# Performance work log

Hardware: AMD Instinct MI355X
Metric: run time of the kernel (lower is better)

Reference implementation:

```python
import jax, jax.numpy as jnp
import numpy as np

S, B, I, H = 512, 64, 512, 512

def setup_inputs() -> dict:
    key = jax.random.key(0)
    ks = jax.random.split(key, 10)
    inp = {
        'x':    jax.random.normal(ks[0], (S, B, I), dtype=jnp.float32),
        'W_xi': jax.random.normal(ks[1], (H, I), dtype=jnp.float32) * (1.0 / np.sqrt(I)),
        'W_hi': jax.random.normal(ks[2], (H, H), dtype=jnp.float32) * (1.0 / np.sqrt(H)),
        'b_i':  jax.random.normal(ks[3], (H,), dtype=jnp.float32),
        'W_xc': jax.random.normal(ks[4], (H, I), dtype=jnp.float32) * (1.0 / np.sqrt(I)),
        'W_hc': jax.random.normal(ks[5], (H, H), dtype=jnp.float32) * (1.0 / np.sqrt(H)),
        'b_c':  jax.random.normal(ks[6], (H,), dtype=jnp.float32),
        'W_xo': jax.random.normal(ks[7], (H, I), dtype=jnp.float32) * (1.0 / np.sqrt(I)),
        'W_ho': jax.random.normal(ks[8], (H, H), dtype=jnp.float32) * (1.0 / np.sqrt(H)),
        'b_o':  jax.random.normal(ks[9], (H,), dtype=jnp.float32),
    }
    return inp

def reference(x, W_xi, W_hi, b_i, W_xc, W_hc, b_c, W_xo, W_ho, b_o):
    seq_len, batch, _ = x.shape
    hidden = W_hi.shape[0]
    # Precompute all input-to-gate projections in one pass: [S,B,H] each
    xi = jnp.einsum('sbi,hi->sbh', x, W_xi)
    xc = jnp.einsum('sbi,hi->sbh', x, W_xc)
    xo = jnp.einsum('sbi,hi->sbh', x, W_xo)

    h0 = jnp.zeros((batch, hidden), dtype=x.dtype)
    c0 = jnp.zeros((batch, hidden), dtype=x.dtype)

    def step(carry, xs):
        h, c = carry
        xi_t, xc_t, xo_t = xs
        i_t = jax.nn.sigmoid(xi_t + h @ W_hi.T + b_i)
        c_hat = jnp.tanh(xc_t + h @ W_hc.T + b_c)
        c = (1.0 - i_t) * c + i_t * c_hat  # coupled forget gate f = 1 - i
        o_t = jax.nn.sigmoid(xo_t + h @ W_ho.T + b_o)
        h = o_t * jnp.tanh(c)
        return (h, c), h

    (h_t, c_t), output = jax.lax.scan(step, (h0, c0), (xi, xc, xo))
    # output: [S,B,H] (time-major, matching torch after transposes)
    return output, h_t, c_t
```

## Files before the change

kernel.cpp:

```cpp
#include <hip/hip_runtime.h>
#include <math.h>

#define SEQ   512
#define BATCH 64
#define HID   512
#define NROW  1536
#define XROW_FLOATS ((size_t)SEQ * NROW * BATCH)
#define HBUF_QWORDS (2 * BATCH * HID)
#define SBH ((size_t)SEQ * BATCH * HID)

__device__ __forceinline__ float sigf(float x) {
    return 1.f / (1.f + __expf(-x));
}
__device__ __forceinline__ float tanh_fast(float x) {
    float ax = fabsf(x);
    float e = __expf(-2.f * ax);
    float r = (1.f - e) / (1.f + e);
    return copysignf(r, x);
}
template <int CTRL>
__device__ __forceinline__ float dpp_add(float v) {
    int x = __builtin_amdgcn_update_dpp(0, __builtin_bit_cast(int, v),
                                        CTRL, 0xf, 0xf, true);
    return v + __builtin_bit_cast(float, x);
}

__global__ __launch_bounds__(256) void xproj_kernel(
    const float* __restrict__ x, const float* __restrict__ Wxi,
    const float* __restrict__ Wxc, const float* __restrict__ Wxo,
    float* __restrict__ xrow)
{
    const int tid = threadIdx.x, lane = tid & 63, wv = tid >> 6;
    const int t = blockIdx.x;
    const int bq = lane & 15;
    const int rq = lane >> 4;
    const float* xb = x + ((size_t)t * 64 + 4 * bq) * 512;

    for (int mm = 0; mm < 12; ++mm) {
        const int R0 = mm * 128 + wv * 32 + rq * 8;
        const int g = R0 >> 9, j0 = R0 & 511;
        const float* wsrc = (g == 0) ? Wxi : ((g == 1) ? Wxc : Wxo);
        const float* wp = wsrc + (size_t)j0 * 512;

        float acc[8][4];
        #pragma unroll
        for (int r = 0; r < 8; ++r)
            #pragma unroll
            for (int j = 0; j < 4; ++j) acc[r][j] = 0.f;

        for (int k4 = 0; k4 < 128; ++k4) {
            float4 xv[4];
            #pragma unroll
            for (int j = 0; j < 4; ++j)
                xv[j] = *(const float4*)(xb + j * 512 + k4 * 4);
            #pragma unroll
            for (int r = 0; r < 8; ++r) {
                const float4 w4 = *(const float4*)(wp + (size_t)r * 512 + k4 * 4);
                #pragma unroll
                for (int j = 0; j < 4; ++j)
                    acc[r][j] += w4.x * xv[j].x + w4.y * xv[j].y
                               + w4.z * xv[j].z + w4.w * xv[j].w;
            }
        }
        #pragma unroll
        for (int r = 0; r < 8; ++r)
            *(float4*)(xrow + ((size_t)t * NROW + R0 + r) * 64 + 4 * bq) =
                make_float4(acc[r][0], acc[r][1], acc[r][2], acc[r][3]);
    }
}

#define HPAD 10
#define H_FLOATS (512 * HPAD)
__global__ __launch_bounds__(512, 2) void scan_kernel(
    const float* __restrict__ xrow,
    const float* __restrict__ Whi, const float* __restrict__ Whc, const float* __restrict__ Who,
    const float* __restrict__ bi, const float* __restrict__ bc, const float* __restrict__ bo,
    unsigned long long* __restrict__ hbuf, float* __restrict__ out)
{
    extern __shared__ float lds[];
    float* hlds = lds;
    float* gbuf = lds + H_FLOATS;
    float* biasL = gbuf + 384;

    const int tid = threadIdx.x, lane = tid & 63;
    const int gid = blockIdx.x & 7;
    const int m   = blockIdx.x >> 3;
    const int rg  = tid >> 5, ks = tid & 31;

    float w3r[16][3];
    #pragma unroll
    for (int r = 0; r < 3; ++r) {
        const int rho = rg * 3 + r;
        const int g = rho >> 4, jloc = rho & 15;
        const float* wsrc = (g == 0) ? Whi : ((g == 1) ? Whc : Who);
        const float* wp = wsrc + (size_t)(m * 16 + jloc) * 512 + ks;
        #pragma unroll
        for (int i = 0; i < 16; ++i) w3r[i][r] = wp[32 * i];
    }
    if (tid < 48) {
        const int g = tid >> 4, jloc = tid & 15;
        const float* bb = (g == 0) ? bi : ((g == 1) ? bc : bo);
        biasL[tid] = bb[m * 16 + jloc];
    }

    const int ejl = tid & 15, eb = tid >> 4;
    const int jg  = m * 16 + ejl;
    const int bg  = gid * 8 + eb;
    float creg = 0.f;

    if (tid < 128) hlds[jg * HPAD + eb] = 0.f;
    __syncthreads();

    const bool own_k = ((tid >> 4) == m);

    for (int t = 0; t < SEQ; ++t) {
        float xr0 = 0.f, xr1 = 0.f, xr2 = 0.f;
        if (tid < 128) {
            const size_t base = ((size_t)t * NROW + jg) * 64 + bg;
            xr0 = xrow[base];
            xr1 = xrow[base + (size_t)512 * 64];
            xr2 = xrow[base + (size_t)1024 * 64];
        }

        if (!own_k) {
            const unsigned long long* hsrc =
                hbuf + (size_t)(t & 1) * (BATCH * HID) + (size_t)gid * 8 * 512 + tid;
            const unsigned tgt = (unsigned)t;
            unsigned long long hv[8];
            #pragma unroll
            for (int q = 0; q < 8; ++q)
                hv[q] = __hip_atomic_load(hsrc + (size_t)q * 512, __ATOMIC_RELAXED,
                                          __HIP_MEMORY_SCOPE_AGENT);
            unsigned pend = 0xffu;
            while (pend) {
                unsigned np = 0;
                #pragma unroll
                for (int q = 0; q < 8; ++q) {
                    if ((pend >> q) & 1) {
                        if ((unsigned)(hv[q] >> 32) >= tgt) {
                            hlds[tid * HPAD + q] =
                                __builtin_bit_cast(float, (unsigned)hv[q]);
                        } else np |= 1u << q;
                    }
                }
                if (np) {
                    #pragma unroll
                    for (int q = 0; q < 8; ++q)
                        if ((np >> q) & 1)
                            hv[q] = __hip_atomic_load(hsrc + (size_t)q * 512,
                                                      __ATOMIC_RELAXED,
                                                      __HIP_MEMORY_SCOPE_AGENT);
                    __builtin_amdgcn_s_sleep(1);
                }
                pend = np;
            }
        }
        __syncthreads();

        float acc[3][8];
        #pragma unroll
        for (int r = 0; r < 3; ++r)
            #pragma unroll
            for (int b = 0; b < 8; ++b) acc[r][b] = 0.f;

        {
            const float* hb = hlds + ks * HPAD;
            #pragma unroll
            for (int i = 0; i < 16; ++i) {
                float hv2[8];
                *(float2*)&hv2[0] = *(const float2*)(hb + i * (32 * HPAD) + 0);
                *(float2*)&hv2[2] = *(const float2*)(hb + i * (32 * HPAD) + 2);
                *(float2*)&hv2[4] = *(const float2*)(hb + i * (32 * HPAD) + 4);
                *(float2*)&hv2[6] = *(const float2*)(hb + i * (32 * HPAD) + 6);
                #pragma unroll
                for (int r = 0; r < 3; ++r)
                    #pragma unroll
                    for (int b = 0; b < 8; ++b)
                        acc[r][b] += w3r[i][r] * hv2[b];
            }
            #pragma unroll
            for (int r = 0; r < 3; ++r)
                #pragma unroll
                for (int b = 0; b < 8; ++b) {
                    float v = acc[r][b];
                    v = dpp_add<0x121>(v);
                    v = dpp_add<0x122>(v);
                    v = dpp_add<0x124>(v);
                    v = dpp_add<0x128>(v);
                    v = dpp_add<0x142>(v);
                    acc[r][b] = v;
                }
            if (lane == 16 || lane == 48) {
                #pragma unroll
                for (int r = 0; r < 3; ++r) {
                    float* gp = gbuf + (rg * 3 + r) * 8;
                    *(float4*)gp       = make_float4(acc[r][0], acc[r][1], acc[r][2], acc[r][3]);
                    *(float4*)(gp + 4) = make_float4(acc[r][4], acc[r][5], acc[r][6], acc[r][7]);
                }
            }
        }
        __syncthreads();

        if (tid < 128) {
            const float pi = xr0 + biasL[ejl]      + gbuf[(0 * 16 + ejl) * 8 + eb];
            const float pc = xr1 + biasL[16 + ejl] + gbuf[(1 * 16 + ejl) * 8 + eb];
            const float po = xr2 + biasL[32 + ejl] + gbuf[(2 * 16 + ejl) * 8 + eb];
            const float it = sigf(pi);
            const float ch = tanh_fast(pc);
            const float ot = sigf(po);
            creg = (1.f - it) * creg + it * ch;
            const float hn = ot * tanh_fast(creg);
            const unsigned long long pv =
                ((unsigned long long)(unsigned)(t + 1) << 32) |
                (unsigned long long)__builtin_bit_cast(unsigned, hn);
            __hip_atomic_store(hbuf + (size_t)((t + 1) & 1) * (BATCH * HID)
                                    + (size_t)bg * 512 + jg,
                               pv, __ATOMIC_RELAXED, __HIP_MEMORY_SCOPE_AGENT);
            hlds[jg * HPAD + eb] = hn;
            out[((size_t)t * 64 + bg) * 512 + jg] = hn;
            if (t == SEQ - 1) {
                out[SBH + (size_t)bg * 512 + jg] = hn;
                out[SBH + 32768 + (size_t)bg * 512 + jg] = creg;
            }
        }
    }
}

extern "C" void kernel_launch(void* const* d_in, const int* in_sizes, int n_in,
                              void* d_out, int out_size, void* d_ws, size_t ws_size,
                              hipStream_t stream)
{
    const float* x   = (const float*)d_in[0];
    const float* Wxi = (const float*)d_in[1];
    const float* Whi = (const float*)d_in[2];
    const float* bi  = (const float*)d_in[3];
    const float* Wxc = (const float*)d_in[4];
    const float* Whc = (const float*)d_in[5];
    const float* bc  = (const float*)d_in[6];
    const float* Wxo = (const float*)d_in[7];
    const float* Who = (const float*)d_in[8];
    const float* bo  = (const float*)d_in[9];
    float* out = (float*)d_out;
    char* ws = (char*)d_ws;

    float*              xrow = (float*)ws;
    unsigned long long* hbuf = (unsigned long long*)(ws + XROW_FLOATS * 4);

    (void)hipMemsetAsync(hbuf, 0, (size_t)HBUF_QWORDS * 8, stream);

    hipLaunchKernelGGL(xproj_kernel, dim3(512), dim3(256), 0, stream,
                       x, Wxi, Wxc, Wxo, xrow);
    hipLaunchKernelGGL(scan_kernel, dim3(256), dim3(512), 22208, stream,
                       xrow, Whi, Whc, Who, bi, bc, bo, hbuf, out);
}
```

Before: 4.798 ms.

## Fuse input projection into scan kernel with producer-consumer counters per timestep

Merges the separate input-projection kernel into the persistent scan kernel. Extra workgroups compute x-projections per timestep slice and publish completion through per-(t,slice) atomic counters, while scan workgroups spin on those counters before reading xrow. This lets the projection GEMM overlap with the sequential recurrence instead of running fully before it. It also moves the hbuf loads ahead of the xrow wait. The risks are contention for CU resources between producer and scan blocks, spin-wait overhead, and a deadlock if not all 512 blocks are co-resident (launch bounds raised to 4 per CU).

```diff
diff --git a/kernel.cpp b/kernel.cpp
--- a/kernel.cpp
+++ b/kernel.cpp
@@ -7,6 +7,7 @@
 #define NROW  1536
 #define XROW_FLOATS ((size_t)SEQ * NROW * BATCH)
 #define HBUF_QWORDS (2 * BATCH * HID)
+#define NCNT  (SEQ * 6)
 #define SBH ((size_t)SEQ * BATCH * HID)
 
 __device__ __forceinline__ float sigf(float x) {
@@ -25,64 +26,85 @@
     return v + __builtin_bit_cast(float, x);
 }
 
-__global__ __launch_bounds__(256) void xproj_kernel(
-    const float* __restrict__ x, const float* __restrict__ Wxi,
-    const float* __restrict__ Wxc, const float* __restrict__ Wxo,
-    float* __restrict__ xrow)
-{
-    const int tid = threadIdx.x, lane = tid & 63, wv = tid >> 6;
-    const int t = blockIdx.x;
-    const int bq = lane & 15;
-    const int rq = lane >> 4;
-    const float* xb = x + ((size_t)t * 64 + 4 * bq) * 512;
-
-    for (int mm = 0; mm < 12; ++mm) {
-        const int R0 = mm * 128 + wv * 32 + rq * 8;
-        const int g = R0 >> 9, j0 = R0 & 511;
-        const float* wsrc = (g == 0) ? Wxi : ((g == 1) ? Wxc : Wxo);
-        const float* wp = wsrc + (size_t)j0 * 512;
-
-        float acc[8][4];
-        #pragma unroll
-        for (int r = 0; r < 8; ++r)
-            #pragma unroll
-            for (int j = 0; j < 4; ++j) acc[r][j] = 0.f;
-
-        for (int k4 = 0; k4 < 128; ++k4) {
-            float4 xv[4];
-            #pragma unroll
-            for (int j = 0; j < 4; ++j)
-                xv[j] = *(const float4*)(xb + j * 512 + k4 * 4);
-            #pragma unroll
-            for (int r = 0; r < 8; ++r) {
-                const float4 w4 = *(const float4*)(wp + (size_t)r * 512 + k4 * 4);
-                #pragma unroll
-                for (int j = 0; j < 4; ++j)
-                    acc[r][j] += w4.x * xv[j].x + w4.y * xv[j].y
-                               + w4.z * xv[j].z + w4.w * xv[j].w;
-            }
-        }
-        #pragma unroll
-        for (int r = 0; r < 8; ++r)
-            *(float4*)(xrow + ((size_t)t * NROW + R0 + r) * 64 + 4 * bq) =
-                make_float4(acc[r][0], acc[r][1], acc[r][2], acc[r][3]);
-    }
-}
-
 #define HPAD 10
 #define H_FLOATS (512 * HPAD)
-__global__ __launch_bounds__(512, 2) void scan_kernel(
-    const float* __restrict__ xrow,
+__global__ __launch_bounds__(512, 4) void fused_kernel(
+    const float* __restrict__ x,
+    const float* __restrict__ Wxi, const float* __restrict__ Wxc, const float* __restrict__ Wxo,
     const float* __restrict__ Whi, const float* __restrict__ Whc, const float* __restrict__ Who,
     const float* __restrict__ bi, const float* __restrict__ bc, const float* __restrict__ bo,
-    unsigned long long* __restrict__ hbuf, float* __restrict__ out)
+    float* __restrict__ xrow, unsigned long long* __restrict__ hbuf,
+    unsigned* __restrict__ cnt, float* __restrict__ out)
 {
     extern __shared__ float lds[];
+    const int tid = threadIdx.x;
+
+    if (blockIdx.x >= 256) {
+        const int xwg  = blockIdx.x - 256;
+        const int wv   = tid >> 6, lane = tid & 63;
+        const int tm   = wv >> 2,  twv  = wv & 3;
+        const int teamid = xwg * 2 + tm;
+        const int bq = lane & 15, rq = lane >> 4;
+
+        for (int round = 0; round < 6; ++round) {
+            const int u = teamid + 512 * round;
+            const int t = u / 6, s = u - 6 * t;
+            const float* xb = x + ((size_t)t * 64 + 4 * bq) * 512;
+
+            for (int half = 0; half < 2; ++half) {
+                const int R0 = s * 256 + half * 128 + twv * 32 + rq * 8;
+                const int g = R0 >> 9, j0 = R0 & 511;
+                const float* wsrc = (g == 0) ? Wxi : ((g == 1) ? Wxc : Wxo);
+                const float* wp = wsrc + (size_t)j0 * 512;
+
+                float acc[8][4];
+                #pragma unroll
+                for (int r = 0; r < 8; ++r)
+                    #pragma unroll
+                    for (int j = 0; j < 4; ++j) acc[r][j] = 0.f;
+
+                for (int k4 = 0; k4 < 128; ++k4) {
+                    float4 xv[4];
+                    #pragma unroll
+                    for (int j = 0; j < 4; ++j)
+                        xv[j] = *(const float4*)(xb + j * 512 + k4 * 4);
+                    #pragma unroll
+                    for (int r = 0; r < 8; ++r) {
+                        const float4 w4 = *(const float4*)(wp + (size_t)r * 512 + k4 * 4);
+                        #pragma unroll
+                        for (int j = 0; j < 4; ++j)
+                            acc[r][j] += w4.x * xv[j].x + w4.y * xv[j].y
+                                       + w4.z * xv[j].z + w4.w * xv[j].w;
+                    }
+                }
+                #pragma unroll
+                for (int r = 0; r < 8; ++r) {
+                    const size_t base = ((size_t)t * NROW + R0 + r) * 64 + 4 * bq;
+                    const unsigned long long p0 =
+                        ((unsigned long long)__builtin_bit_cast(unsigned, acc[r][1]) << 32) |
+                        __builtin_bit_cast(unsigned, acc[r][0]);
+                    const unsigned long long p1 =
+                        ((unsigned long long)__builtin_bit_cast(unsigned, acc[r][3]) << 32) |
+                        __builtin_bit_cast(unsigned, acc[r][2]);
+                    __hip_atomic_store((unsigned long long*)(xrow + base), p0,
+                                       __ATOMIC_RELAXED, __HIP_MEMORY_SCOPE_AGENT);
+                    __hip_atomic_store((unsigned long long*)(xrow + base) + 1, p1,
+                                       __ATOMIC_RELAXED, __HIP_MEMORY_SCOPE_AGENT);
+                }
+            }
+            __builtin_amdgcn_s_waitcnt(0);
+            if (lane == 0)
+                __hip_atomic_fetch_add(cnt + t * 6 + s, 1u,
+                                       __ATOMIC_RELAXED, __HIP_MEMORY_SCOPE_AGENT);
+        }
+        return;
+    }
+
     float* hlds = lds;
     float* gbuf = lds + H_FLOATS;
     float* biasL = gbuf + 384;
 
-    const int tid = threadIdx.x, lane = tid & 63;
+    const int lane = tid & 63;
     const int gid = blockIdx.x & 7;
     const int m   = blockIdx.x >> 3;
     const int rg  = tid >> 5, ks = tid & 31;
@@ -106,6 +128,7 @@
     const int ejl = tid & 15, eb = tid >> 4;
     const int jg  = m * 16 + ejl;
     const int bg  = gid * 8 + eb;
+    const int s0  = m >> 4;
     float creg = 0.f;
 
     if (tid < 128) hlds[jg * HPAD + eb] = 0.f;
@@ -114,23 +137,39 @@
     const bool own_k = ((tid >> 4) == m);
 
     for (int t = 0; t < SEQ; ++t) {
-        float xr0 = 0.f, xr1 = 0.f, xr2 = 0.f;
-        if (tid < 128) {
-            const size_t base = ((size_t)t * NROW + jg) * 64 + bg;
-            xr0 = xrow[base];
-            xr1 = xrow[base + (size_t)512 * 64];
-            xr2 = xrow[base + (size_t)1024 * 64];
-        }
-
+        const unsigned long long* hsrc =
+            hbuf + (size_t)(t & 1) * (BATCH * HID) + (size_t)gid * 8 * 512 + tid;
+        unsigned long long hv[8];
         if (!own_k) {
-            const unsigned long long* hsrc =
-                hbuf + (size_t)(t & 1) * (BATCH * HID) + (size_t)gid * 8 * 512 + tid;
-            const unsigned tgt = (unsigned)t;
-            unsigned long long hv[8];
             #pragma unroll
             for (int q = 0; q < 8; ++q)
                 hv[q] = __hip_atomic_load(hsrc + (size_t)q * 512, __ATOMIC_RELAXED,
                                           __HIP_MEMORY_SCOPE_AGENT);
+        }
+
+        float xr0 = 0.f, xr1 = 0.f, xr2 = 0.f;
+        if (tid < 128) {
+            const unsigned* cb = cnt + t * 6 + s0;
+            unsigned c0 = __hip_atomic_load(cb,     __ATOMIC_RELAXED, __HIP_MEMORY_SCOPE_AGENT);
+            unsigned c1 = __hip_atomic_load(cb + 2, __ATOMIC_RELAXED, __HIP_MEMORY_SCOPE_AGENT);
+            unsigned c2 = __hip_atomic_load(cb + 4, __ATOMIC_RELAXED, __HIP_MEMORY_SCOPE_AGENT);
+            while (!(c0 >= 4u && c1 >= 4u && c2 >= 4u)) {
+                c0 = __hip_atomic_load(cb,     __ATOMIC_RELAXED, __HIP_MEMORY_SCOPE_AGENT);
+                c1 = __hip_atomic_load(cb + 2, __ATOMIC_RELAXED, __HIP_MEMORY_SCOPE_AGENT);
+                c2 = __hip_atomic_load(cb + 4, __ATOMIC_RELAXED, __HIP_MEMORY_SCOPE_AGENT);
+                __builtin_amdgcn_s_sleep(1);
+            }
+            const size_t base = ((size_t)t * NROW + jg) * 64 + bg;
+            xr0 = __builtin_bit_cast(float, __hip_atomic_load(
+                (const unsigned*)xrow + base, __ATOMIC_RELAXED, __HIP_MEMORY_SCOPE_AGENT));
+            xr1 = __builtin_bit_cast(float, __hip_atomic_load(
+                (const unsigned*)xrow + base + (size_t)512 * 64, __ATOMIC_RELAXED, __HIP_MEMORY_SCOPE_AGENT));
+            xr2 = __builtin_bit_cast(float, __hip_atomic_load(
+                (const unsigned*)xrow + base + (size_t)1024 * 64, __ATOMIC_RELAXED, __HIP_MEMORY_SCOPE_AGENT));
+        }
+
+        if (!own_k) {
+            const unsigned tgt = (unsigned)t;
             unsigned pend = 0xffu;
             while (pend) {
                 unsigned np = 0;
@@ -245,11 +284,11 @@
 
     float*              xrow = (float*)ws;
     unsigned long long* hbuf = (unsigned long long*)(ws + XROW_FLOATS * 4);
-
-    (void)hipMemsetAsync(hbuf, 0, (size_t)HBUF_QWORDS * 8, stream);
-
-    hipLaunchKernelGGL(xproj_kernel, dim3(512), dim3(256), 0, stream,
-                       x, Wxi, Wxc, Wxo, xrow);
-    hipLaunchKernelGGL(scan_kernel, dim3(256), dim3(512), 22208, stream,
-                       xrow, Whi, Whc, Who, bi, bc, bo, hbuf, out);
-}
+    unsigned*           cnt  = (unsigned*)(ws + XROW_FLOATS * 4 + (size_t)HBUF_QWORDS * 8);
+
+    (void)hipMemsetAsync(hbuf, 0, (size_t)HBUF_QWORDS * 8 + (size_t)NCNT * 4, stream);
+
+    hipLaunchKernelGGL(fused_kernel, dim3(512), dim3(512), 22208, stream,
+                       x, Wxi, Wxc, Wxo, Whi, Whc, Who, bi, bc, bo,
+                       xrow, hbuf, cnt, out);
+}
```

Result: slower. 7.644 ms (+59.3%).
